# Kernel tuning notes

Hardware: AMD Instinct MI355X
Metric: run time of the kernel (lower is better)

## Reference

```python
import jax, jax.numpy as jnp
import numpy as np

NEG = -1e9
NP_N, EP = 30000, 480000
NL, EL, T = 48, 144, 96
NA, D = 11, 256
I_STOP = NL
PHI = 1 + 5 * D + 4 * NA
VAL_VEC = jnp.array([4., 1., 3., 1., 2., 1., 5., 1., 6., 1., 1000.], dtype=jnp.float32)
BOND_VAL = jnp.array([1., 2., 3., 1.5], dtype=jnp.float32)


def gcn2(x, src, dst, w, W1, b1, W2, b2):
    # two-layer GCN with symmetric norm + self loops (PyG GCNConv semantics)
    n = x.shape[0]
    loops = jnp.arange(n, dtype=src.dtype)
    s = jnp.concatenate([src, loops])
    d = jnp.concatenate([dst, loops])
    ww = jnp.concatenate([w, jnp.ones((n,), x.dtype)])
    deg = jax.ops.segment_sum(ww, d, num_segments=n)
    dinv = jnp.where(deg > 0, deg ** -0.5, 0.0)
    norm = (ww * dinv[s] * dinv[d])[:, None]
    def conv(h, W, b):
        return jax.ops.segment_sum((h @ W)[s] * norm, d, num_segments=n) + b
    return conv(jax.nn.relu(conv(x, W1, b1)), W2, b2)


def _forward(x_p, x_l_geom, Wp1, bp1, Wp2, bp2, Wl1, bl1, Wl2, bl2,
             Wd1, bd1, Wd2, bd2, Wf, bf, Wg, bg, Wh, bh,
             src_p, dst_p, src_l, dst_l, x_l_label, bfs_index, bfs_bond):
    f32, i32 = jnp.float32, jnp.int32
    src_p = src_p.astype(i32); dst_p = dst_p.astype(i32)
    src_l = src_l.astype(i32); dst_l = dst_l.astype(i32)
    bfs_index = bfs_index.astype(i32); bfs_bond = bfs_bond.astype(i32)
    x_l_label = x_l_label.astype(i32)
    x_l = jnp.concatenate([x_l_geom, jax.nn.one_hot(x_l_label, NA, dtype=f32)], 1)
    z_pocket = gcn2(x_p, src_p, dst_p, jnp.ones((EP,), f32), Wp1, bp1, Wp2, bp2).mean(0)
    z_l = gcn2(x_l, src_l, dst_l, jnp.ones((EL,), f32), Wl1, bl1, Wl2, bl2)
    lab_true = x_l[:, 4:]
    # f: atom label classifier, teacher-forced log prob of true labels
    lmask = jnp.zeros((NA,), f32).at[-1].set(NEG)
    logp = jax.nn.log_softmax(z_l @ Wf + bf + lmask, -1)[jnp.arange(NL), x_l_label].sum()
    H_init = jnp.concatenate([z_l, lab_true], 1).mean(0)
    lab_v = jnp.concatenate([lab_true, jax.nn.one_hot(jnp.array([NA - 1]), NA, dtype=f32)], 0)  # append Stop node
    e0 = bfs_index[0]
    z_v0 = gcn2(lab_v, e0[:1], e0[1:2], jnp.ones((1,), f32), Wd1, bd1, Wd2, bd2)
    H_t0 = jnp.concatenate([z_v0, lab_v], 1).mean(0)
    val0 = lab_v @ VAL_VEC
    N1 = NL + 1
    E = 2 * T
    Q0 = jnp.zeros((T + 1,), i32).at[0].set(bfs_index[0, 0])
    carry0 = (jnp.asarray(0.0, f32), val0, jnp.zeros((N1,), bool), jnp.zeros((N1, N1), bool),
              jnp.zeros((E,), i32), jnp.zeros((E,), i32), jnp.zeros((E,), bool), jnp.asarray(0, i32),
              Q0, jnp.asarray(0, i32), jnp.asarray(1, i32), z_v0, H_t0, jnp.asarray(0.0, f32))

    def step(carry, xs):
        logp, val, closed, adj, esrc, edst, evalid, ec, Q, head, tail, z_v, H_t, time = carry
        v, bidx = xs
        active = tail > head
        u = Q[head]
        phi = jnp.concatenate([
            jnp.full((N1, 1), time, f32),
            jnp.broadcast_to(z_pocket, (N1, D)),
            jnp.broadcast_to(z_v[u], (N1, D)),
            jnp.broadcast_to(lab_v[u], (N1, NA)),
            z_v, lab_v,
            jnp.broadcast_to(H_t, (N1, D + NA)),
            jnp.broadcast_to(H_init, (N1, D + NA))], 1)
        # node mask (valency / closed / already-bonded / self), then unmask {v, stop}
        base = jnp.where((val < 1) | closed | adj[u], NEG, 0.0).at[u].set(NEG)
        m_nou = jnp.where(val[u] < 1, jnp.full((N1,), NEG, f32), base)
        m = m_nou.at[v].set(0.0).at[I_STOP].set(0.0)
        glog = (phi @ Wg + bg)[:, 0] + m
        logp = logp + jnp.where(active, jax.nn.log_softmax(glog)[v], 0.0)
        is_stop = v == I_STOP
        pop = active & is_stop
        do_edge = active & (~is_stop)
        closed = closed.at[u].set(jnp.where(pop, True, closed[u]))
        head = head + pop.astype(jnp.int32)
        Q = Q.at[tail].set(jnp.where(do_edge, v, Q[tail]), mode='drop')
        tail = tail + do_edge.astype(jnp.int32)
        esrc = esrc.at[ec].set(u, mode='drop').at[ec + 1].set(v, mode='drop')
        edst = edst.at[ec].set(v, mode='drop').at[ec + 1].set(u, mode='drop')
        evalid = evalid.at[ec].set(do_edge, mode='drop').at[ec + 1].set(do_edge, mode='drop')
        ec = ec + 2 * do_edge.astype(jnp.int32)
        # bond mask row on min valency of (u, v)
        mv = jnp.minimum(val[u], val[v])
        two = jnp.array([0., 0., NEG, 0.], f32)
        one = jnp.array([0., NEG, NEG, 0.], f32)
        zer = jnp.full((4,), NEG, f32)
        e = jnp.where(mv <= 2, two, jnp.zeros((4,), f32))
        e = jnp.where(mv <= 1, one, e)
        e = jnp.where(mv <= 0, zer, e)
        e = jnp.where(m_nou[v] <= NEG * 0.5, zer, e)
        e = e.at[bidx].set(0.0)  # unmask true bond
        hlog = phi[v] @ Wh + bh + e
        logp = logp + jnp.where(do_edge, jax.nn.log_softmax(hlog)[bidx], 0.0)
        dec = jnp.where(do_edge, BOND_VAL[bidx], 0.0)
        val = val.at[u].add(-dec).at[v].add(-dec)
        adj = adj.at[u, v].set(jnp.where(do_edge, True, adj[u, v])).at[v, u].set(jnp.where(do_edge, True, adj[v, u]))
        z_new = gcn2(lab_v, esrc, edst, evalid.astype(f32), Wd1, bd1, Wd2, bd2)
        z_v = jnp.where(do_edge, z_new, z_v)
        H_t = jnp.where(do_edge, jnp.concatenate([z_new, lab_v], 1).mean(0), H_t)
        time = time + do_edge.astype(f32)
        return (logp, val, closed, adj, esrc, edst, evalid, ec, Q, head, tail, z_v, H_t, time), None

    carry, _ = jax.lax.scan(step, carry0, (bfs_index[:, 1], bfs_bond))
    return carry[0]


def setup_inputs():
    key = jax.random.key(0)
    ks = jax.random.split(key, 30)
    f32 = jnp.float32
    def w(i, shape):
        return jax.random.normal(ks[i], shape, f32) * 0.05
    inp = {}
    inp['x_p'] = jax.random.normal(ks[0], (NP_N, 15), f32)
    inp['src_p'] = jax.random.randint(ks[1], (EP,), 0, NP_N)
    inp['dst_p'] = jax.random.randint(ks[2], (EP,), 0, NP_N)
    inp['x_l_geom'] = jax.random.normal(ks[3], (NL, 4), f32)
    inp['x_l_label'] = jax.random.randint(ks[4], (NL,), 0, NA - 1)
    inp['src_l'] = jax.random.randint(ks[5], (EL,), 0, NL)
    inp['dst_l'] = jax.random.randint(ks[6], (EL,), 0, NL)
    inp['bfs_index'] = jax.random.randint(ks[7], (T, 2), 0, NL + 1)
    inp['bfs_bond'] = jax.random.randint(ks[8], (T,), 0, 4)
    inp['Wp1'] = w(9, (15, D)); inp['bp1'] = w(10, (D,))
    inp['Wp2'] = w(11, (D, D)); inp['bp2'] = w(12, (D,))
    inp['Wl1'] = w(13, (15, D)); inp['bl1'] = w(14, (D,))
    inp['Wl2'] = w(15, (D, D)); inp['bl2'] = w(16, (D,))
    inp['Wd1'] = w(17, (NA, D)); inp['bd1'] = w(18, (D,))
    inp['Wd2'] = w(19, (D, D)); inp['bd2'] = w(20, (D,))
    inp['Wf'] = w(21, (D, NA)); inp['bf'] = w(22, (NA,))
    inp['Wg'] = w(23, (PHI, 1)); inp['bg'] = w(24, (1,))
    inp['Wh'] = w(25, (PHI, 4)); inp['bh'] = w(26, (4,))
    return inp


def reference(x_p, src_p, dst_p, x_l_geom, x_l_label, src_l, dst_l, bfs_index, bfs_bond,
              Wp1, bp1, Wp2, bp2, Wl1, bl1, Wl2, bl2, Wd1, bd1, Wd2, bd2,
              Wf, bf, Wg, bg, Wh, bh):
    return _forward(x_p, x_l_geom, Wp1, bp1, Wp2, bp2, Wl1, bl1, Wl2, bl2,
                    Wd1, bd1, Wd2, bd2, Wf, bf, Wg, bg, Wh, bh,
                    src_p, dst_p, src_l, dst_l, x_l_label, bfs_index, bfs_bond)
```

## Files before the change

### kernel.cpp

```cpp
#include <hip/hip_runtime.h>
#include <math.h>

#define NPn 30000
#define EPn 480000
#define NLl 48
#define ELl 144
#define Tn 96
#define NAn 11
#define Dn 256
#define N1 49
#define NEGf (-1000000000.0f)
#define NSTATES 97
#define CHN 125
#define PC 13
#define YN (N1*PC)


__global__ __launch_bounds__(256) void kA(
    const int* __restrict__ dst_p, int* __restrict__ deg,
    const int* __restrict__ lab_in, const int* __restrict__ bfs_i, const int* __restrict__ bfs_b,
    int* __restrict__ lab_idx, float* __restrict__ lab_means,
    int* __restrict__ dirs, int* __restrict__ dird, float* __restrict__ m_arr,
    float* __restrict__ e_arr, int* __restrict__ rec, int* __restrict__ Sout,
    const float* __restrict__ xg, const int* __restrict__ srcl, const int* __restrict__ dstl,
    const float* __restrict__ Wl1, const float* __restrict__ bl1,
    const float* __restrict__ Wl2, const float* __restrict__ bl2, float* __restrict__ zl_mean,
    const float* __restrict__ Wd2, const float* __restrict__ Wg, const float* __restrict__ Wh,
    float* __restrict__ Pm){
  const int bid = blockIdx.x;
  const int tid = threadIdx.x;

  if (bid == 0){
    if (tid >= 64) return;
    const int lane = tid;
    int vA = bfs_i[2*lane+1];
    int vB = (lane<Tn-64)? bfs_i[2*(64+lane)+1] : 0;
    int bA = bfs_b[lane];
    int bB = (lane<Tn-64)? bfs_b[64+lane] : 0;
    int labv = (lane<NLl)? lab_in[lane] : (NAn-1);
    float val_r;
    switch(labv){
      case 0: val_r=4.f; break; case 1: val_r=1.f; break; case 2: val_r=3.f; break;
      case 3: val_r=1.f; break; case 4: val_r=2.f; break; case 5: val_r=1.f; break;
      case 6: val_r=5.f; break; case 7: val_r=1.f; break; case 8: val_r=6.f; break;
      case 9: val_r=1.f; break; default: val_r=1000.f; break;
    }
    if (lane<N1) lab_idx[lane]=labv;
    for (int a=0;a<NAn;a++){
      unsigned long long mask = __ballot(lane<NLl && labv==a);
      int cnt = __popcll(mask);
      if (lane==a){
        lab_means[a]     = ((float)cnt + ((a==NAn-1)?1.f:0.f))*(1.0f/49.0f);
        lab_means[NAn+a] = (float)cnt*(1.0f/48.0f);
      }
    }
    int closed_r = 0;
    unsigned long long adjmask = 0ull;
    int q0 = 0, q1 = 0;
    int e0s = bfs_i[0], e0d = bfs_i[1];
    if (lane==0){ q0 = e0s; dirs[192]=e0s; dird[192]=e0d; }
    int head=0, tail=1, ec=0, timec=0;
    for (int t=0;t<Tn;t++){
      int v   = (t<64)? __shfl(vA,t) : __shfl(vB,t-64);
      int bix = (t<64)? __shfl(bA,t) : __shfl(bB,t-64);
      int active = (tail>head)?1:0;
      int u = (head<64)? __shfl(q0,head) : __shfl(q1,head-64);
      float valu = __shfl(val_r,u);
      float valv = __shfl(val_r,v);
      float base = (val_r<1.f || closed_r || ((adjmask>>u)&1ull)) ? NEGf : 0.f;
      if (lane==u) base=NEGf;
      float mnou = (valu<1.f)? NEGf : base;
      float m = mnou;
      if (lane==v) m=0.f;
      if (lane==NLl) m=0.f;
      if (lane<N1) m_arr[t*N1+lane]=m;
      float mnv = __shfl(mnou,v);
      if (lane<4){
        float mv = fminf(valu,valv);
        float e;
        if (mv<=0.f) e=NEGf;
        else if (mv<=1.f) e=((lane==1)||(lane==2))?NEGf:0.f;
        else if (mv<=2.f) e=(lane==2)?NEGf:0.f;
        else e=0.f;
        if (mnv <= NEGf*0.5f) e=NEGf;
        if (lane==bix) e=0.f;
        e_arr[t*4+lane]=e;
      }
      int is_stop = (v==NLl)?1:0;
      int pop = active & is_stop;
      int doe = active & (is_stop^1);
      if (lane==0){
        rec[t]=u; rec[Tn+t]=v; rec[2*Tn+t]=bix; rec[3*Tn+t]=active; rec[4*Tn+t]=doe; rec[5*Tn+t]=timec;
      }
      if (doe){
        if (tail<64){ if (lane==tail) q0=v; }
        else        { if (lane==tail-64) q1=v; }
        if (lane==0){ dirs[ec]=u; dird[ec]=v; dirs[ec+1]=v; dird[ec+1]=u; }
        float dec = (bix==0)?1.f:(bix==1)?2.f:(bix==2)?3.f:1.5f;
        if (lane==u) val_r-=dec;
        if (lane==v) val_r-=dec;
        if (lane==u) adjmask |= (1ull<<v);
        if (lane==v) adjmask |= (1ull<<u);
      }
      if (pop && lane==u) closed_r=1;
      head+=pop; tail+=doe; ec+=2*doe; timec+=doe;
    }
    if (lane==0) Sout[0]=ec/2;
    return;
  }

  if (bid == 1){
    __shared__ float sW[15*Dn];
    __shared__ float svec[NLl*4];
    __shared__ float scnt[NLl*11];
    __shared__ float ow[NLl];
    __shared__ float rs[Dn];
    __shared__ float sdinv[NLl];
    __shared__ int sdeg[NLl];
    __shared__ int ses[ELl], sed[ELl];
    __shared__ int slab[NLl];
    if (tid<NLl){ sdeg[tid]=1; slab[tid]=lab_in[tid]; }
    for (int i=tid;i<NLl*4;i+=256) svec[i]=0.f;
    for (int i=tid;i<NLl*11;i+=256) scnt[i]=0.f;
    for (int i=tid;i<15*Dn;i+=256) sW[i]=Wl1[i];
    __syncthreads();
    if (tid<ELl){ ses[tid]=srcl[tid]; sed[tid]=dstl[tid]; atomicAdd(&sdeg[dstl[tid]],1); }
    __syncthreads();
    if (tid<NLl) sdinv[tid]=rsqrtf((float)sdeg[tid]);
    __syncthreads();
    if (tid<NLl){
      float dv=sdinv[tid];
      ow[tid]=dv;
      for (int q=0;q<4;q++) svec[tid*4+q]=xg[tid*4+q]*dv;
      scnt[tid*11+slab[tid]]=dv;
    }
    __syncthreads();
    if (tid<ELl){
      int s=ses[tid], d=sed[tid];
      float dvs=sdinv[s];
      for (int q=0;q<4;q++) atomicAdd(&svec[d*4+q], xg[s*4+q]*dvs);
      atomicAdd(&scnt[d*11+slab[s]], dvs);
      atomicAdd(&ow[s], sdinv[d]);
    }
    __syncthreads();
    {
      int c=tid;
      float b=bl1[c];
      float rsum=0.f;
      for (int d=0;d<NLl;d++){
        float a=0.f;
        for (int q=0;q<4;q++)  a=fmaf(svec[d*4+q], sW[q*Dn+c], a);
        for (int aa=0;aa<11;aa++) a=fmaf(scnt[d*11+aa], sW[(4+aa)*Dn+c], a);
        float h=fmaxf(sdinv[d]*a + b, 0.f);
        rsum = fmaf(sdinv[d]*ow[d], h, rsum);
      }
      rs[c]=rsum*(1.0f/48.0f);
    }
    __syncthreads();
    {
      int c=tid;
      float a=0.f;
      for (int k=0;k<Dn;k++) a=fmaf(rs[k], Wl2[(size_t)k*Dn+c], a);
      zl_mean[c]=a+bl2[c];
    }
    return;
  }

  if (bid < 2+64){
    const int lane = tid&63, wv = tid>>6;
    const int k = (bid-2)*4 + wv;
    float pg=0.f;
    float4 pu=make_float4(0,0,0,0), pv=make_float4(0,0,0,0), ph=make_float4(0,0,0,0);
    for (int q=0;q<4;q++){
      int n = lane + 64*q;
      float w = Wd2[(size_t)k*Dn+n];
      pg = fmaf(w, Wg[524+n], pg);
      float4 a=*(const float4*)&Wh[(size_t)(257+n)*4];
      float4 b=*(const float4*)&Wh[(size_t)(524+n)*4];
      float4 c=*(const float4*)&Wh[(size_t)(791+n)*4];
      pu.x=fmaf(w,a.x,pu.x); pu.y=fmaf(w,a.y,pu.y); pu.z=fmaf(w,a.z,pu.z); pu.w=fmaf(w,a.w,pu.w);
      pv.x=fmaf(w,b.x,pv.x); pv.y=fmaf(w,b.y,pv.y); pv.z=fmaf(w,b.z,pv.z); pv.w=fmaf(w,b.w,pv.w);
      ph.x=fmaf(w,c.x,ph.x); ph.y=fmaf(w,c.y,ph.y); ph.z=fmaf(w,c.z,ph.z); ph.w=fmaf(w,c.w,ph.w);
    }
    for (int off=32; off>0; off>>=1){
      pg += __shfl_xor(pg,off);
      pu.x+=__shfl_xor(pu.x,off); pu.y+=__shfl_xor(pu.y,off); pu.z+=__shfl_xor(pu.z,off); pu.w+=__shfl_xor(pu.w,off);
      pv.x+=__shfl_xor(pv.x,off); pv.y+=__shfl_xor(pv.y,off); pv.z+=__shfl_xor(pv.z,off); pv.w+=__shfl_xor(pv.w,off);
      ph.x+=__shfl_xor(ph.x,off); ph.y+=__shfl_xor(ph.y,off); ph.z+=__shfl_xor(ph.z,off); ph.w+=__shfl_xor(ph.w,off);
    }
    if (lane==0){
      float* o = Pm + k*PC;
      o[0]=pg; o[1]=pu.x; o[2]=pu.y; o[3]=pu.z; o[4]=pu.w;
      o[5]=pv.x; o[6]=pv.y; o[7]=pv.z; o[8]=pv.w;
      o[9]=ph.x; o[10]=ph.y; o[11]=ph.z; o[12]=ph.w;
    }
    return;
  }

  {
    int e = (bid-66)*256 + tid;
    if (e < EPn) atomicAdd(&deg[dst_p[e]], 1);
  }
}


__global__ void k_xagg(const int* __restrict__ src, const int* __restrict__ dst,
                       const float* __restrict__ xp, const int* __restrict__ deg,
                       float* __restrict__ xagg, float* __restrict__ odegw){
  int g = blockIdx.x*blockDim.x + threadIdx.x;
  int e = g>>4, c = g&15;
  if (e >= EPn) return;
  int s = src[e], d = dst[e];
  if (c < 15){
    float dvs = rsqrtf((float)(deg[s]+1));
    atomicAdd(&xagg[d*16+c], xp[s*15+c]*dvs);
  } else {
    float dvd = rsqrtf((float)(deg[d]+1));
    atomicAdd(&odegw[s], dvd);
  }
}

__global__ __launch_bounds__(256) void k_fuse(const float* __restrict__ xp, const float* __restrict__ xagg,
    const int* __restrict__ deg, const float* __restrict__ odegw,
    const float* __restrict__ Wp1, const float* __restrict__ bp1, float* __restrict__ zr){
  __shared__ float sx[CHN][16];
  __shared__ float sc[CHN];
  int tid = threadIdx.x;
  int base = blockIdx.x*CHN;
  float wcol[15];
  for (int k=0;k<15;k++) wcol[k]=Wp1[k*Dn+tid];
  float b = bp1[tid];
  for (int i=tid;i<CHN*16;i+=256){
    int n = base+(i>>4), c = i&15;
    float v = 0.f;
    if (n<NPn && c<15){
      float dv = rsqrtf((float)(deg[n]+1));
      v = (xagg[n*16+c] + xp[n*15+c]*dv)*dv;
    }
    sx[i>>4][i&15]=v;
  }
  for (int i=tid;i<CHN;i+=256){
    int n = base+i;
    float dv = (n<NPn)? rsqrtf((float)(deg[n]+1)) : 0.f;
    sc[i] = (n<NPn)? dv*(odegw[n]+dv) : 0.f;
  }
  __syncthreads();
  float acc = 0.f;
  int lim = (NPn-base < CHN)? (NPn-base) : CHN;
  for (int i=0;i<lim;i++){
    float d0 = b;
    for (int k=0;k<15;k++) d0 = fmaf(sx[i][k], wcol[k], d0);
    acc = fmaf(sc[i], fmaxf(d0,0.f), acc);
  }
  atomicAdd(&zr[tid], acc);
}


__global__ __launch_bounds__(256) void k_zh(const float* __restrict__ zr, const float* __restrict__ Wp2,
    const float* __restrict__ bp2, const float* __restrict__ zl, const float* __restrict__ lm,
    const float* __restrict__ b2, const float* __restrict__ Wh, const float* __restrict__ bh,
    float* __restrict__ hc4){
  __shared__ float sr[Dn];
  __shared__ float zp[Dn];
  int tid=threadIdx.x;
  sr[tid]=zr[tid]*(1.0f/30000.0f);
  __syncthreads();
  float a=0.f;
  for (int k=0;k<Dn;k++) a=fmaf(sr[k],Wp2[(size_t)k*Dn+tid],a);
  zp[tid]=a+bp2[tid];
  __syncthreads();
  if (tid<64){
    int lane=tid;
    float4 h=make_float4(0,0,0,0);
    for (int q=0;q<4;q++){
      int n=lane+64*q;
      float4 w1=*(const float4*)&Wh[(size_t)(1+n)*4];
      float4 w2=*(const float4*)&Wh[(size_t)(1058+n)*4];
      float4 wu=*(const float4*)&Wh[(size_t)(257+n)*4];
      float4 wv=*(const float4*)&Wh[(size_t)(524+n)*4];
      float4 wh=*(const float4*)&Wh[(size_t)(791+n)*4];
      float zpn=zp[n], zln=zl[n], bn=b2[n];
      h.x += zpn*w1.x + zln*w2.x + bn*(wu.x+wv.x+wh.x);
      h.y += zpn*w1.y + zln*w2.y + bn*(wu.y+wv.y+wh.y);
      h.z += zpn*w1.z + zln*w2.z + bn*(wu.z+wv.z+wh.z);
      h.w += zpn*w1.w + zln*w2.w + bn*(wu.w+wv.w+wh.w);
    }
    if (lane<NAn){
      float4 wa=*(const float4*)&Wh[(size_t)(1047+lane)*4];
      float4 wb=*(const float4*)&Wh[(size_t)(1314+lane)*4];
      float aa=lm[lane], bb=lm[NAn+lane];
      h.x += aa*wa.x + bb*wb.x; h.y += aa*wa.y + bb*wb.y;
      h.z += aa*wa.z + bb*wb.z; h.w += aa*wa.w + bb*wb.w;
    }
    for (int off=32; off>0; off>>=1){
      h.x+=__shfl_xor(h.x,off); h.y+=__shfl_xor(h.y,off);
      h.z+=__shfl_xor(h.z,off); h.w+=__shfl_xor(h.w,off);
    }
    if (lane==0){
      hc4[0]=h.x+bh[0]; hc4[1]=h.y+bh[1]; hc4[2]=h.z+bh[2]; hc4[3]=h.w+bh[3];
    }
  }
}


__global__ __launch_bounds__(256) void k_dc(const int* __restrict__ Sp, const int* __restrict__ dirs,
    const int* __restrict__ dird, const int* __restrict__ lab_idx,
    const float* __restrict__ Wd1, const float* __restrict__ bd1,
    const float* __restrict__ Pm, const int* __restrict__ rec,
    const float* __restrict__ m_arr, const float* __restrict__ e_arr,
    const float* __restrict__ hc4, const float* __restrict__ Wg, const float* __restrict__ Wh,
    float* __restrict__ out){
  int k = blockIdx.x;
  if (k > Sp[0]) return;
  __shared__ float sW[11*Dn];
  __shared__ float sP[Dn*PC];
  __shared__ float hT[Dn*N1];
  __shared__ float cnt[N1*11];
  __shared__ float y1[YN];
  __shared__ float za[YN];
  __shared__ float sdinv[N1];
  __shared__ int sdeg[N1];
  __shared__ int se[192], sd[192];
  __shared__ int slab[N1];
  __shared__ int srec[6*Tn];
  int tid=threadIdx.x;
  int ecnt = (k==0)?1:(2*k);
  int base = (k==0)?192:0;
  if (tid<N1){ sdeg[tid]=1; slab[tid]=lab_idx[tid]; }
  for (int i=tid;i<N1*11;i+=256) cnt[i]=0.f;
  for (int i=tid;i<11*Dn;i+=256) sW[i]=Wd1[i];
  for (int i=tid;i<Dn*PC;i+=256) sP[i]=Pm[i];
  for (int i=tid;i<6*Tn;i+=256) srec[i]=rec[i];
  __syncthreads();
  if (tid<ecnt){ se[tid]=dirs[base+tid]; sd[tid]=dird[base+tid]; atomicAdd(&sdeg[sd[tid]],1); }
  __syncthreads();
  if (tid<N1) sdinv[tid]=rsqrtf((float)sdeg[tid]);
  __syncthreads();
  if (tid<N1) cnt[tid*11+slab[tid]] = sdinv[tid];
  __syncthreads();
  if (tid<ecnt) atomicAdd(&cnt[sd[tid]*11+slab[se[tid]]], sdinv[se[tid]]);
  __syncthreads();
  {
    int c=tid;
    float wreg[11];
    for (int a=0;a<11;a++) wreg[a]=sW[a*Dn+c];
    float b=bd1[c];
    for (int r=0;r<N1;r++){
      float s=0.f;
      for (int a=0;a<11;a++) s=fmaf(cnt[r*11+a], wreg[a], s);
      hT[c*N1+r]=fmaxf(sdinv[r]*s + b, 0.f);
    }
  }
  __syncthreads();
  for (int idx=tid; idx<YN; idx+=256){
    int r=idx/PC, j=idx-r*PC;
    float acc=0.f;
    for (int c=0;c<Dn;c++) acc=fmaf(hT[c*N1+r], sP[c*PC+j], acc);
    y1[idx]=acc;
    za[idx]=sdinv[r]*acc;
  }
  __syncthreads();
  for (int i=tid; i<ecnt*PC; i+=256){
    int e=i/PC, j=i-e*PC;
    atomicAdd(&za[sd[e]*PC+j], sdinv[se[e]]*y1[se[e]*PC+j]);
  }
  __syncthreads();
  for (int idx=tid; idx<YN; idx+=256){
    int r=idx/PC;
    za[idx]=sdinv[r]*za[idx];
  }
  __syncthreads();
  if (tid>=64) return;
  const int lane=tid;
  for (int t=0;t<Tn;t++){
    if (!srec[3*Tn+t] || srec[5*Tn+t]!=k) continue;
    const int u=srec[t], v=srec[Tn+t], bidx=srec[2*Tn+t], doe=srec[4*Tn+t];
    float g = -INFINITY;
    float4 hm = make_float4(0,0,0,0);
    if (lane<N1){
      const float* zrow = za + lane*PC;
      g = zrow[0] + Wg[780+slab[lane]] + m_arr[t*N1+lane];
      hm.x=zrow[9]; hm.y=zrow[10]; hm.z=zrow[11]; hm.w=zrow[12];
    }
    float gv = __shfl(g, v);
    float gM = g;
    for (int off=32; off>0; off>>=1) gM = fmaxf(gM, __shfl_xor(gM, off));
    float ex = (lane<N1)? expf(g-gM) : 0.f;
    float gS = ex;
    for (int off=32; off>0; off>>=1){
      gS += __shfl_xor(gS, off);
      hm.x+=__shfl_xor(hm.x,off); hm.y+=__shfl_xor(hm.y,off);
      hm.z+=__shfl_xor(hm.z,off); hm.w+=__shfl_xor(hm.w,off);
    }
    if (lane==0){
      float res = gv - gM - logf(gS);
      if (doe){
        const int lu=slab[u], lv=slab[v];
        const float tf=(float)k;
        float h[4];
        for (int j=0;j<4;j++){
          float hmj = (j==0)?hm.x:(j==1)?hm.y:(j==2)?hm.z:hm.w;
          h[j] = hc4[j] + tf*Wh[j] + Wh[(513+lu)*4+j] + Wh[(780+lv)*4+j]
               + za[u*PC+1+j] + za[v*PC+5+j] + hmj*(1.0f/49.0f) + e_arr[4*t+j];
        }
        float M=fmaxf(fmaxf(h[0],h[1]),fmaxf(h[2],h[3]));
        float se2=expf(h[0]-M)+expf(h[1]-M)+expf(h[2]-M)+expf(h[3]-M);
        float hb=(bidx==0)?h[0]:(bidx==1)?h[1]:(bidx==2)?h[2]:h[3];
        res += hb - M - logf(se2);
      }
      atomicAdd(out, res);
    }
  }
}


extern "C" void kernel_launch(void* const* d_in, const int* in_sizes, int n_in,
                              void* d_out, int out_size, void* d_ws, size_t ws_size,
                              hipStream_t stream){
  const float* x_p      =(const float*)d_in[0];
  const int*   src_p    =(const int*)d_in[1];
  const int*   dst_p    =(const int*)d_in[2];
  const float* x_l_geom =(const float*)d_in[3];
  const int*   x_l_label=(const int*)d_in[4];
  const int*   src_l    =(const int*)d_in[5];
  const int*   dst_l    =(const int*)d_in[6];
  const int*   bfs_index=(const int*)d_in[7];
  const int*   bfs_bond =(const int*)d_in[8];
  const float* Wp1=(const float*)d_in[9];
  const float* bp1=(const float*)d_in[10];
  const float* Wp2=(const float*)d_in[11];
  const float* bp2=(const float*)d_in[12];
  const float* Wl1=(const float*)d_in[13];
  const float* bl1=(const float*)d_in[14];
  const float* Wl2=(const float*)d_in[15];
  const float* bl2=(const float*)d_in[16];
  const float* Wd1=(const float*)d_in[17];
  const float* bd1=(const float*)d_in[18];
  const float* Wd2=(const float*)d_in[19];
  const float* bd2=(const float*)d_in[20];
  const float* Wg =(const float*)d_in[23];
  const float* Wh =(const float*)d_in[25];
  const float* bh =(const float*)d_in[26];

  char* w=(char*)d_ws;
  size_t off=0;
  auto alloc=[&](size_t bytes)->char*{ char* p=w+off; off=(off+bytes+255)&~((size_t)255); return p; };
  int*   deg    =(int*)alloc((size_t)NPn*4);
  float* odegw  =(float*)alloc((size_t)NPn*4);
  float* xagg   =(float*)alloc((size_t)NPn*16*4);
  float* zr     =(float*)alloc(Dn*4);
  size_t zero_span = off;
  float* zl_mean=(float*)alloc(Dn*4);
  float* Pm     =(float*)alloc(Dn*PC*4);
  float* hc4    =(float*)alloc(4*4);
  float* m_arr  =(float*)alloc((size_t)Tn*N1*4);
  float* e_arr  =(float*)alloc((size_t)Tn*4*4);
  int*   rec    =(int*)alloc((size_t)6*Tn*4);
  int*   dirs   =(int*)alloc(194*4);
  int*   dird   =(int*)alloc(194*4);
  int*   lab_idx=(int*)alloc(N1*4);
  float* lab_means=(float*)alloc(2*NAn*4);
  int*   Sval   =(int*)alloc(4);
  (void)in_sizes;(void)n_in;(void)ws_size;

  hipMemsetAsync(d_ws, 0, zero_span, stream);
  hipMemsetAsync(d_out, 0, (size_t)out_size*sizeof(float), stream);

  kA<<<66 + EPn/256, 256, 0, stream>>>(
      dst_p, deg,
      x_l_label, bfs_index, bfs_bond, lab_idx, lab_means, dirs, dird, m_arr, e_arr, rec, Sval,
      x_l_geom, src_l, dst_l, Wl1, bl1, Wl2, bl2, zl_mean,
      Wd2, Wg, Wh, Pm);
  k_xagg<<<EPn*16/256,256,0,stream>>>(src_p,dst_p,x_p,deg,xagg,odegw);
  k_fuse<<<(NPn+CHN-1)/CHN,256,0,stream>>>(x_p,xagg,deg,odegw,Wp1,bp1,zr);
  k_zh<<<1,256,0,stream>>>(zr,Wp2,bp2,zl_mean,lab_means,bd2,Wh,bh,hc4);
  k_dc<<<NSTATES,256,0,stream>>>(Sval,dirs,dird,lab_idx,Wd1,bd1,Pm,rec,m_arr,e_arr,hc4,Wg,Wh,(float*)d_out);
}
```

Before: 285.7 us.

## Split BFS simulation in block 0 into scalar queue pass and parallel mask passes

Block 0's single-wave BFS replay, which built the queue, the per-lane valence state and the mask outputs in one serial loop full of shuffles, is split into phases. Thread 0 first runs the cheap queue/head/tail recurrence into shared arrays. All 96 steps then write rec/dirs in parallel, and one wave replays only the valence/adjacency state into a shared base table. Finally all four waves write m_arr and e_arr in parallel. This shortens the serial critical path of block 0 at the cost of more shared memory and a few extra barriers.

```diff
diff --git a/kernel.cpp b/kernel.cpp
--- a/kernel.cpp
+++ b/kernel.cpp
@@ -31,81 +31,115 @@
   const int tid = threadIdx.x;
 
   if (bid == 0){
-    if (tid >= 64) return;
-    const int lane = tid;
-    int vA = bfs_i[2*lane+1];
-    int vB = (lane<Tn-64)? bfs_i[2*(64+lane)+1] : 0;
-    int bA = bfs_b[lane];
-    int bB = (lane<Tn-64)? bfs_b[64+lane] : 0;
-    int labv = (lane<NLl)? lab_in[lane] : (NAn-1);
-    float val_r;
-    switch(labv){
-      case 0: val_r=4.f; break; case 1: val_r=1.f; break; case 2: val_r=3.f; break;
-      case 3: val_r=1.f; break; case 4: val_r=2.f; break; case 5: val_r=1.f; break;
-      case 6: val_r=5.f; break; case 7: val_r=1.f; break; case 8: val_r=6.f; break;
-      case 9: val_r=1.f; break; default: val_r=1000.f; break;
-    }
-    if (lane<N1) lab_idx[lane]=labv;
-    for (int a=0;a<NAn;a++){
-      unsigned long long mask = __ballot(lane<NLl && labv==a);
-      int cnt = __popcll(mask);
-      if (lane==a){
-        lab_means[a]     = ((float)cnt + ((a==NAn-1)?1.f:0.f))*(1.0f/49.0f);
-        lab_means[NAn+a] = (float)cnt*(1.0f/48.0f);
-      }
-    }
-    int closed_r = 0;
-    unsigned long long adjmask = 0ull;
-    int q0 = 0, q1 = 0;
-    int e0s = bfs_i[0], e0d = bfs_i[1];
-    if (lane==0){ q0 = e0s; dirs[192]=e0s; dird[192]=e0d; }
-    int head=0, tail=1, ec=0, timec=0;
-    for (int t=0;t<Tn;t++){
-      int v   = (t<64)? __shfl(vA,t) : __shfl(vB,t-64);
-      int bix = (t<64)? __shfl(bA,t) : __shfl(bB,t-64);
-      int active = (tail>head)?1:0;
-      int u = (head<64)? __shfl(q0,head) : __shfl(q1,head-64);
-      float valu = __shfl(val_r,u);
-      float valv = __shfl(val_r,v);
-      float base = (val_r<1.f || closed_r || ((adjmask>>u)&1ull)) ? NEGf : 0.f;
-      if (lane==u) base=NEGf;
-      float mnou = (valu<1.f)? NEGf : base;
-      float m = mnou;
-      if (lane==v) m=0.f;
-      if (lane==NLl) m=0.f;
-      if (lane<N1) m_arr[t*N1+lane]=m;
-      float mnv = __shfl(mnou,v);
-      if (lane<4){
-        float mv = fminf(valu,valv);
-        float e;
-        if (mv<=0.f) e=NEGf;
-        else if (mv<=1.f) e=((lane==1)||(lane==2))?NEGf:0.f;
-        else if (mv<=2.f) e=(lane==2)?NEGf:0.f;
-        else e=0.f;
-        if (mnv <= NEGf*0.5f) e=NEGf;
-        if (lane==bix) e=0.f;
-        e_arr[t*4+lane]=e;
-      }
-      int is_stop = (v==NLl)?1:0;
-      int pop = active & is_stop;
-      int doe = active & (is_stop^1);
-      if (lane==0){
-        rec[t]=u; rec[Tn+t]=v; rec[2*Tn+t]=bix; rec[3*Tn+t]=active; rec[4*Tn+t]=doe; rec[5*Tn+t]=timec;
-      }
-      if (doe){
-        if (tail<64){ if (lane==tail) q0=v; }
-        else        { if (lane==tail-64) q1=v; }
-        if (lane==0){ dirs[ec]=u; dird[ec]=v; dirs[ec+1]=v; dird[ec+1]=u; }
-        float dec = (bix==0)?1.f:(bix==1)?2.f:(bix==2)?3.f:1.5f;
-        if (lane==u) val_r-=dec;
-        if (lane==v) val_r-=dec;
-        if (lane==u) adjmask |= (1ull<<v);
-        if (lane==v) adjmask |= (1ull<<u);
-      }
-      if (pop && lane==u) closed_r=1;
-      head+=pop; tail+=doe; ec+=2*doe; timec+=doe;
-    }
-    if (lane==0) Sout[0]=ec/2;
+    __shared__ int sv[Tn], sb[Tn];
+    __shared__ int qarr[Tn+1];
+    __shared__ int uArr[Tn], headA[Tn], doeA[Tn], popA[Tn], actA[Tn], timeA[Tn], eidxA[Tn];
+    __shared__ float decA[Tn], valuA[Tn], valvA[Tn];
+    __shared__ float baseB[Tn][N1];
+    __shared__ int slab[N1];
+    __shared__ int cntL[NAn];
+    if (tid < Tn){ sv[tid]=bfs_i[2*tid+1]; sb[tid]=bfs_b[tid]; }
+    if (tid <= Tn) qarr[tid]=0;
+    if (tid < NAn) cntL[tid]=0;
+    if (tid < N1){ int l=(tid<NLl)? lab_in[tid] : (NAn-1); slab[tid]=l; lab_idx[tid]=l; }
+    __syncthreads();
+    if (tid < NLl) atomicAdd(&cntL[slab[tid]],1);
+    if (tid == 0) qarr[0]=bfs_i[0];
+    __syncthreads();
+    if (tid < NAn){
+      int c=cntL[tid];
+      lab_means[tid]     = ((float)c + ((tid==NAn-1)?1.f:0.f))*(1.0f/49.0f);
+      lab_means[NAn+tid] = (float)c*(1.0f/48.0f);
+    }
+    if (tid == 0){
+      dirs[192]=qarr[0]; dird[192]=bfs_i[1];
+      int head=0, tail=1, ec=0, timec=0;
+      for (int t=0;t<Tn;t++){
+        int v = sv[t];
+        int active = (tail>head)?1:0;
+        int is_stop = (v==NLl)?1:0;
+        int pop = active & is_stop;
+        int doe = active & (is_stop^1);
+        headA[t]=head; actA[t]=active; doeA[t]=doe; popA[t]=pop; timeA[t]=timec;
+        eidxA[t] = doe ? ec : -1;
+        int bix = sb[t];
+        decA[t] = (bix==0)?1.f:(bix==1)?2.f:(bix==2)?3.f:1.5f;
+        if (doe && tail<=Tn) qarr[tail]=v;
+        head+=pop; tail+=doe; ec+=2*doe; timec+=doe;
+      }
+      Sout[0]=ec/2;
+    }
+    __syncthreads();
+    if (tid < Tn){
+      int t=tid;
+      int h=headA[t]; if (h>Tn) h=Tn;
+      int u=qarr[h];
+      uArr[t]=u;
+      rec[t]=u; rec[Tn+t]=sv[t]; rec[2*Tn+t]=sb[t];
+      rec[3*Tn+t]=actA[t]; rec[4*Tn+t]=doeA[t]; rec[5*Tn+t]=timeA[t];
+      int ei=eidxA[t];
+      if (ei>=0 && ei<192){
+        int v=sv[t];
+        dirs[ei]=u; dird[ei]=v; dirs[ei+1]=v; dird[ei+1]=u;
+      }
+    }
+    __syncthreads();
+    if (tid < 64){
+      const int l = tid;
+      int labv = (l<N1)? slab[l] : 0;
+      float val;
+      switch(labv){
+        case 0: val=4.f; break; case 1: val=1.f; break; case 2: val=3.f; break;
+        case 3: val=1.f; break; case 4: val=2.f; break; case 5: val=1.f; break;
+        case 6: val=5.f; break; case 7: val=1.f; break; case 8: val=6.f; break;
+        case 9: val=1.f; break; default: val=1000.f; break;
+      }
+      if (l>=N1) val=0.f;
+      int closed=0;
+      unsigned long long adjm=0ull;
+      for (int t=0;t<Tn;t++){
+        int u=uArr[t], v=sv[t];
+        int doe=doeA[t], pop=popA[t];
+        float base = (val<1.f || closed || ((adjm>>u)&1ull)) ? NEGf : 0.f;
+        if (l==u) base=NEGf;
+        if (l<N1) baseB[t][l]=base;
+        if (l==u) valuA[t]=val;
+        if (l==v) valvA[t]=val;
+        if (doe){
+          float dec=decA[t];
+          if (l==u){ val-=dec; adjm |= (1ull<<v); }
+          if (l==v){ val-=dec; adjm |= (1ull<<u); }
+        }
+        if (pop && l==u) closed=1;
+      }
+    }
+    __syncthreads();
+    {
+      const int lane=tid&63, wv=tid>>6;
+      for (int t=wv; t<Tn; t+=4){
+        float valu=valuA[t], valv=valvA[t];
+        int v=sv[t], bix=sb[t];
+        if (lane<N1){
+          float mnou = (valu<1.f)? NEGf : baseB[t][lane];
+          float m = mnou;
+          if (lane==v) m=0.f;
+          if (lane==NLl) m=0.f;
+          m_arr[t*N1+lane]=m;
+        }
+        if (lane<4){
+          float mnv = (valu<1.f)? NEGf : baseB[t][v];
+          float mv = fminf(valu,valv);
+          float e;
+          if (mv<=0.f) e=NEGf;
+          else if (mv<=1.f) e=((lane==1)||(lane==2))?NEGf:0.f;
+          else if (mv<=2.f) e=(lane==2)?NEGf:0.f;
+          else e=0.f;
+          if (mnv <= NEGf*0.5f) e=NEGf;
+          if (lane==bix) e=0.f;
+          e_arr[t*4+lane]=e;
+        }
+      }
+    }
     return;
   }
 
@@ -118,8 +152,8 @@
     __shared__ float sdinv[NLl];
     __shared__ int sdeg[NLl];
     __shared__ int ses[ELl], sed[ELl];
-    __shared__ int slab[NLl];
-    if (tid<NLl){ sdeg[tid]=1; slab[tid]=lab_in[tid]; }
+    __shared__ int slab2[NLl];
+    if (tid<NLl){ sdeg[tid]=1; slab2[tid]=lab_in[tid]; }
     for (int i=tid;i<NLl*4;i+=256) svec[i]=0.f;
     for (int i=tid;i<NLl*11;i+=256) scnt[i]=0.f;
     for (int i=tid;i<15*Dn;i+=256) sW[i]=Wl1[i];
@@ -132,14 +166,14 @@
       float dv=sdinv[tid];
       ow[tid]=dv;
       for (int q=0;q<4;q++) svec[tid*4+q]=xg[tid*4+q]*dv;
-      scnt[tid*11+slab[tid]]=dv;
+      scnt[tid*11+slab2[tid]]=dv;
     }
     __syncthreads();
     if (tid<ELl){
       int s=ses[tid], d=sed[tid];
       float dvs=sdinv[s];
       for (int q=0;q<4;q++) atomicAdd(&svec[d*4+q], xg[s*4+q]*dvs);
-      atomicAdd(&scnt[d*11+slab[s]], dvs);
+      atomicAdd(&scnt[d*11+slab2[s]], dvs);
       atomicAdd(&ow[s], sdinv[d]);
     }
     __syncthreads();
```

New measurement: 273.5 us. 4.3% less time.
